# Optimization experiments

Measured on AMD Instinct MI355X. Metric: run time of the kernel, lower is better.

## Reference

```python
import jax, jax.numpy as jnp
import numpy as np

TAYLOR_ORDER = 16      # Taylor terms after scaling (||A_s|| <= 0.5 -> machine precision)
MAX_SQUARINGS = 16     # fixed upper bound on squaring steps (jit-friendly)


def batched_expm(A):
    """Vectorized scaling-and-squaring matrix exponential for A of shape [..., n, n].

    Replaces the original per-item torch.linalg.matrix_exp Python loop with one
    fused batched computation (same math: exp(Q*t)).
    """
    n = A.shape[-1]
    I = jnp.eye(n, dtype=A.dtype)
    # per-matrix infinity norm [...,]
    nrm = jnp.max(jnp.sum(jnp.abs(A), axis=-1), axis=-1)
    # number of squarings so that scaled norm <= 0.5
    s = jnp.clip(jnp.ceil(jnp.log2(jnp.maximum(nrm, 1e-30) / 0.5)), 0.0, float(MAX_SQUARINGS))
    As = A * jnp.exp2(-s)[..., None, None]
    # Taylor series: P = I + As + As^2/2! + ...
    P = jnp.broadcast_to(I, A.shape)
    term = P
    for k in range(1, TAYLOR_ORDER + 1):
        term = jnp.matmul(term, As) / k
        P = P + term
    # undo scaling: square s times (data-dependent count via masked squaring)
    s_b = s[..., None, None]
    for i in range(MAX_SQUARINGS):
        P = jnp.where(s_b > i, jnp.matmul(P, P), P)
    return P


def setup_inputs() -> dict:
    key = jax.random.key(0)
    k1, k2 = jax.random.split(key)
    rate_matrix = jax.random.normal(k1, (64, 32768, 4, 4), dtype=jnp.float32)
    time = jax.random.uniform(k2, (64,), dtype=jnp.float32)
    return {"rate_matrix": rate_matrix, "time": time}


def reference(rate_matrix, time):
    # Qt = rate_matrix[i, j] * time[i], batched over (batch, seq_len)
    Qt = rate_matrix * time[:, None, None, None]
    return batched_expm(Qt)  # [B, S, 4, 4] transition probability matrices
```

## Files before the change

### kernel.cpp

```cpp
#include <hip/hip_runtime.h>
#include <math.h>


constexpr int TAYLOR_N = 10;

__global__ void __launch_bounds__(256) expm4_kernel(
    const float* __restrict__ A,
    const float* __restrict__ tvec,
    float* __restrict__ out,
    int M, int S)
{
    const int m = blockIdx.x * 256 + threadIdx.x;
    if (m >= M) return;

    const float t = tvec[m / S];

    float a[16];
    const float4* Ap = reinterpret_cast<const float4*>(A) + (size_t)m * 4;
    #pragma unroll
    for (int i = 0; i < 4; ++i) {
        float4 v = Ap[i];
        a[4*i+0] = v.x * t;
        a[4*i+1] = v.y * t;
        a[4*i+2] = v.z * t;
        a[4*i+3] = v.w * t;
    }

    float nrm = 0.0f;
    #pragma unroll
    for (int i = 0; i < 4; ++i) {
        float rs = fabsf(a[4*i+0]) + fabsf(a[4*i+1])
                 + fabsf(a[4*i+2]) + fabsf(a[4*i+3]);
        nrm = fmaxf(nrm, rs);
    }

    float sf = ceilf(log2f(fmaxf(nrm, 1e-30f) * 2.0f));
    sf = fminf(fmaxf(sf, 0.0f), 16.0f);
    const int   si    = (int)sf;
    const float scale = exp2f(-sf);
    #pragma unroll
    for (int i = 0; i < 16; ++i) a[i] *= scale;

    float P[16], T[16];
    #pragma unroll
    for (int i = 0; i < 16; ++i) { T[i] = a[i]; P[i] = a[i]; }
    P[0] += 1.0f; P[5] += 1.0f; P[10] += 1.0f; P[15] += 1.0f;

    #pragma unroll
    for (int k = 2; k <= TAYLOR_N; ++k) {
        const float rk = 1.0f / (float)k;
        #pragma unroll
        for (int i = 0; i < 4; ++i) {
            const float t0 = T[4*i+0], t1 = T[4*i+1];
            const float t2 = T[4*i+2], t3 = T[4*i+3];
            #pragma unroll
            for (int j = 0; j < 4; ++j) {
                float v = t0*a[j] + t1*a[4+j] + t2*a[8+j] + t3*a[12+j];
                v *= rk;
                T[4*i+j] = v;
                P[4*i+j] += v;
            }
        }
    }

    for (int it = 0; it < si; ++it) {
        float Q[16];
        #pragma unroll
        for (int i = 0; i < 4; ++i) {
            const float p0 = P[4*i+0], p1 = P[4*i+1];
            const float p2 = P[4*i+2], p3 = P[4*i+3];
            #pragma unroll
            for (int j = 0; j < 4; ++j) {
                Q[4*i+j] = p0*P[j] + p1*P[4+j] + p2*P[8+j] + p3*P[12+j];
            }
        }
        #pragma unroll
        for (int i = 0; i < 16; ++i) P[i] = Q[i];
    }

    float4* Op = reinterpret_cast<float4*>(out) + (size_t)m * 4;
    #pragma unroll
    for (int i = 0; i < 4; ++i) {
        float4 v;
        v.x = P[4*i+0]; v.y = P[4*i+1]; v.z = P[4*i+2]; v.w = P[4*i+3];
        Op[i] = v;
    }
}

extern "C" void kernel_launch(void* const* d_in, const int* in_sizes, int n_in,
                              void* d_out, int out_size, void* d_ws, size_t ws_size,
                              hipStream_t stream) {
    const float* A    = (const float*)d_in[0];
    const float* tvec = (const float*)d_in[1];
    float* out        = (float*)d_out;

    const int B = in_sizes[1];
    const int M = in_sizes[0] / 16;
    const int S = M / B;

    const int threads = 256;
    const int blocks  = (M + threads - 1) / threads;
    expm4_kernel<<<blocks, threads, 0, stream>>>(A, tvec, out, M, S);
}
```

Baseline: 231.9 us.

## Evaluate degree-9 Taylor via Paterson-Stockmeyer and unroll squaring loop by two

```diff
diff --git a/kernel.cpp b/kernel.cpp
--- a/kernel.cpp
+++ b/kernel.cpp
@@ -2,7 +2,26 @@
 #include <math.h>
 
 
-constexpr int TAYLOR_N = 10;
+typedef float f4 __attribute__((ext_vector_type(4)));
+
+__device__ __forceinline__ void mm4(float* __restrict__ D,
+                                    const float* __restrict__ X,
+                                    const float* __restrict__ Y)
+{
+    #pragma unroll
+    for (int i = 0; i < 4; ++i) {
+        const float x0 = X[4*i+0], x1 = X[4*i+1];
+        const float x2 = X[4*i+2], x3 = X[4*i+3];
+        #pragma unroll
+        for (int j = 0; j < 4; ++j) {
+            float v = x0 * Y[j];
+            v = __builtin_fmaf(x1, Y[4+j],  v);
+            v = __builtin_fmaf(x2, Y[8+j],  v);
+            v = __builtin_fmaf(x3, Y[12+j], v);
+            D[4*i+j] = v;
+        }
+    }
+}
 
 __global__ void __launch_bounds__(256) expm4_kernel(
     const float* __restrict__ A,
@@ -16,10 +35,10 @@
     const float t = tvec[m / S];
 
     float a[16];
-    const float4* Ap = reinterpret_cast<const float4*>(A) + (size_t)m * 4;
+    const f4* Ap = reinterpret_cast<const f4*>(A) + (size_t)m * 4;
     #pragma unroll
     for (int i = 0; i < 4; ++i) {
-        float4 v = Ap[i];
+        f4 v = Ap[i];
         a[4*i+0] = v.x * t;
         a[4*i+1] = v.y * t;
         a[4*i+2] = v.z * t;
@@ -41,49 +60,79 @@
     #pragma unroll
     for (int i = 0; i < 16; ++i) a[i] *= scale;
 
-    float P[16], T[16];
+    float A2[16], A3[16];
+    mm4(A2, a, a);
+    mm4(A3, A2, a);
+
+    constexpr float C2 = 1.0f/2.0f,    C3 = 1.0f/6.0f;
+    constexpr float C4 = 1.0f/24.0f,   C5 = 1.0f/120.0f;
+    constexpr float C6 = 1.0f/720.0f,  C7 = 1.0f/5040.0f;
+    constexpr float C8 = 1.0f/40320.0f, C9 = 1.0f/362880.0f;
+
+    float G[16], HI[16], PI[16];
     #pragma unroll
-    for (int i = 0; i < 16; ++i) { T[i] = a[i]; P[i] = a[i]; }
-    P[0] += 1.0f; P[5] += 1.0f; P[10] += 1.0f; P[15] += 1.0f;
+    for (int i = 0; i < 16; ++i) {
+        G[i]  = __builtin_fmaf(C9, A3[i],
+                __builtin_fmaf(C8, A2[i], C7 * a[i]));
+        HI[i] = __builtin_fmaf(C5, A2[i], C4 * a[i]);
+        PI[i] = __builtin_fmaf(C2, A2[i], a[i]);
+    }
+    G[0]  += C6; G[5]  += C6; G[10] += C6; G[15] += C6;
+    HI[0] += C3; HI[5] += C3; HI[10] += C3; HI[15] += C3;
+    PI[0] += 1.0f; PI[5] += 1.0f; PI[10] += 1.0f; PI[15] += 1.0f;
 
+    float H[16];
     #pragma unroll
-    for (int k = 2; k <= TAYLOR_N; ++k) {
-        const float rk = 1.0f / (float)k;
+    for (int i = 0; i < 4; ++i) {
+        const float g0 = G[4*i+0], g1 = G[4*i+1];
+        const float g2 = G[4*i+2], g3 = G[4*i+3];
         #pragma unroll
-        for (int i = 0; i < 4; ++i) {
-            const float t0 = T[4*i+0], t1 = T[4*i+1];
-            const float t2 = T[4*i+2], t3 = T[4*i+3];
-            #pragma unroll
-            for (int j = 0; j < 4; ++j) {
-                float v = t0*a[j] + t1*a[4+j] + t2*a[8+j] + t3*a[12+j];
-                v *= rk;
-                T[4*i+j] = v;
-                P[4*i+j] += v;
-            }
+        for (int j = 0; j < 4; ++j) {
+            float v = HI[4*i+j];
+            v = __builtin_fmaf(g0, A3[j],    v);
+            v = __builtin_fmaf(g1, A3[4+j],  v);
+            v = __builtin_fmaf(g2, A3[8+j],  v);
+            v = __builtin_fmaf(g3, A3[12+j], v);
+            H[4*i+j] = v;
         }
     }
 
-    for (int it = 0; it < si; ++it) {
+    float P[16];
+    #pragma unroll
+    for (int i = 0; i < 4; ++i) {
+        const float h0 = H[4*i+0], h1 = H[4*i+1];
+        const float h2 = H[4*i+2], h3 = H[4*i+3];
+        #pragma unroll
+        for (int j = 0; j < 4; ++j) {
+            float v = PI[4*i+j];
+            v = __builtin_fmaf(h0, A3[j],    v);
+            v = __builtin_fmaf(h1, A3[4+j],  v);
+            v = __builtin_fmaf(h2, A3[8+j],  v);
+            v = __builtin_fmaf(h3, A3[12+j], v);
+            P[4*i+j] = v;
+        }
+    }
+
+    int it = si;
+    while (it >= 2) {
         float Q[16];
-        #pragma unroll
-        for (int i = 0; i < 4; ++i) {
-            const float p0 = P[4*i+0], p1 = P[4*i+1];
-            const float p2 = P[4*i+2], p3 = P[4*i+3];
-            #pragma unroll
-            for (int j = 0; j < 4; ++j) {
-                Q[4*i+j] = p0*P[j] + p1*P[4+j] + p2*P[8+j] + p3*P[12+j];
-            }
-        }
+        mm4(Q, P, P);
+        mm4(P, Q, Q);
+        it -= 2;
+    }
+    if (it) {
+        float Q[16];
+        mm4(Q, P, P);
         #pragma unroll
         for (int i = 0; i < 16; ++i) P[i] = Q[i];
     }
 
-    float4* Op = reinterpret_cast<float4*>(out) + (size_t)m * 4;
+    f4* Op = reinterpret_cast<f4*>(out) + (size_t)m * 4;
     #pragma unroll
     for (int i = 0; i < 4; ++i) {
-        float4 v;
+        f4 v;
         v.x = P[4*i+0]; v.y = P[4*i+1]; v.z = P[4*i+2]; v.w = P[4*i+3];
-        Op[i] = v;
+        __builtin_nontemporal_store(v, Op + i);
     }
 }
 
```

Result: slower. 280.5 us (+20.9%).
